# Optimization experiments

Measured on AMD Instinct MI355X. Metric: run time of the kernel, lower is better.

Reference implementation:

```python
import jax, jax.numpy as jnp
import numpy as np

E = 8        # n_experts
H = 1024     # hidden
F = 1024     # ffn intermediate
K = 2        # top_k
B, T = 2, 1024


def setup_inputs() -> dict:
    key = jax.random.key(0)
    k1, k2, k3, k4 = jax.random.split(key, 4)
    return {
        "hidden_states": jax.random.normal(k1, (B, T, H), dtype=jnp.float32),
        "router_weight": jax.random.normal(k2, (E, H), dtype=jnp.float32),
        "gate_up_proj": jax.random.normal(k3, (E, 2 * F, H), dtype=jnp.float32),
        "down_proj": jax.random.normal(k4, (E, H, F), dtype=jnp.float32),
    }


def reference(hidden_states, router_weight, gate_up_proj, down_proj):
    b, t, h_dim = hidden_states.shape
    h = hidden_states.reshape(-1, h_dim)                      # [N, H]

    # Router: logits -> softmax -> top-k -> renormalize (matches FakeFusedRouter)
    logits = h @ router_weight.T                              # [N, E]
    probs = jax.nn.softmax(logits, axis=-1)
    top_v, top_i = jax.lax.top_k(probs, K)                    # [N, K]
    top_v = top_v / top_v.sum(axis=-1, keepdims=True)

    # Combine weights per expert: w[e, n] = sum_k top_v[n,k] * [top_i[n,k]==e]
    combine = (jax.nn.one_hot(top_i, E, dtype=top_v.dtype) * top_v[..., None]).sum(axis=1)  # [N, E]
    combine = combine.T                                       # [E, N]

    # Scan over experts: each expert runs its SwiGLU FFN over all tokens,
    # masked/weighted by combine (zero weight == token not routed there).
    def body(acc, xs):
        gu, dp, w = xs                                        # [2F,H], [H,F], [N]
        gate, up = jnp.split(h @ gu.T, 2, axis=-1)            # [N,F] each
        out = (jax.nn.silu(gate) * up) @ dp.T                 # [N,H]
        return acc + w[:, None] * out, None

    acc0 = jnp.zeros_like(h)
    final, _ = jax.lax.scan(body, acc0, (gate_up_proj, down_proj, combine))
    return final.reshape(b, t, h_dim)
```

## Files before the change

### kernel.cpp

```cpp
#include <hip/hip_runtime.h>


#define NTOK   2048
#define HDIM   1024
#define FDIM   1024
#define NEXP   8
#define NKROWS 4096
#define MAXTILES 40

typedef __attribute__((ext_vector_type(8))) __bf16 bf16x8;
typedef __attribute__((ext_vector_type(4))) float  floatx4;

__device__ __forceinline__ unsigned short f2bf(float x) {
    unsigned int u = __builtin_bit_cast(unsigned int, x);
    u += 0x7FFFu + ((u >> 16) & 1u);
    return (unsigned short)(u >> 16);
}

__device__ __forceinline__ float bf2f(unsigned short v) {
    unsigned int u = (unsigned int)v << 16;
    return __builtin_bit_cast(float, u);
}

__device__ __forceinline__ bf16x8 cvt8(float4 a, float4 b) {
    bf16x8 r;
    r[0] = (__bf16)a.x; r[1] = (__bf16)a.y; r[2] = (__bf16)a.z; r[3] = (__bf16)a.w;
    r[4] = (__bf16)b.x; r[5] = (__bf16)b.y; r[6] = (__bf16)b.z; r[7] = (__bf16)b.w;
    return r;
}

__device__ __forceinline__ void dma16(const void* g, void* l) {
    __builtin_amdgcn_global_load_lds(
        (const __attribute__((address_space(1))) unsigned int*)g,
        (__attribute__((address_space(3))) unsigned int*)l, 16, 0, 0);
}

__global__ __launch_bounds__(256) void k_router(
    const float* __restrict__ h, const float* __restrict__ rw,
    unsigned short* __restrict__ hbf,
    int* __restrict__ topk_idx, float* __restrict__ topk_w)
{
    const int lane = threadIdx.x & 63;
    const int wave = threadIdx.x >> 6;
    const int n = blockIdx.x * 4 + wave;

    const float4* hp = reinterpret_cast<const float4*>(h + (size_t)n * HDIM);
    uint2* hb = reinterpret_cast<uint2*>(hbf + (size_t)n * HDIM);
    float acc[NEXP];
#pragma unroll
    for (int e = 0; e < NEXP; ++e) acc[e] = 0.f;

#pragma unroll
    for (int i0 = 0; i0 < HDIM / 4; i0 += 64) {
        float4 hv = hp[i0 + lane];
        uint2 o;
        o.x = (unsigned)f2bf(hv.x) | ((unsigned)f2bf(hv.y) << 16);
        o.y = (unsigned)f2bf(hv.z) | ((unsigned)f2bf(hv.w) << 16);
        hb[i0 + lane] = o;
#pragma unroll
        for (int e = 0; e < NEXP; ++e) {
            float4 rv = reinterpret_cast<const float4*>(rw + e * HDIM)[i0 + lane];
            acc[e] += hv.x * rv.x + hv.y * rv.y + hv.z * rv.z + hv.w * rv.w;
        }
    }
#pragma unroll
    for (int e = 0; e < NEXP; ++e) {
#pragma unroll
        for (int off = 32; off > 0; off >>= 1)
            acc[e] += __shfl_xor(acc[e], off);
    }
    if (lane == 0) {
        int i0 = 0; float m0 = acc[0];
        for (int e = 1; e < NEXP; ++e) if (acc[e] > m0) { m0 = acc[e]; i0 = e; }
        int i1 = -1; float m1 = -3.0e38f;
        for (int e = 0; e < NEXP; ++e) if (e != i0 && acc[e] > m1) { m1 = acc[e]; i1 = e; }
        float d  = __expf(m1 - m0);
        float w0 = 1.f / (1.f + d);
        topk_idx[n * 2 + 0] = i0;
        topk_idx[n * 2 + 1] = i1;
        topk_w [n * 2 + 0] = w0;
        topk_w [n * 2 + 1] = 1.f - w0;
    }
}

__global__ __launch_bounds__(256) void k_build_perm(
    const int* __restrict__ topk_idx, const float* __restrict__ topk_w,
    int* __restrict__ offsets, int* __restrict__ perm_slot, float* __restrict__ row_w,
    int* __restrict__ tile_e, int* __restrict__ tile_rt)
{
    __shared__ int cnt[NEXP];
    __shared__ int cur[NEXP];
    __shared__ int off[NEXP + 1];
    const int t = threadIdx.x;
    if (t < NEXP) cnt[t] = 0;
    __syncthreads();
    for (int s = t; s < NKROWS; s += 256) atomicAdd(&cnt[topk_idx[s]], 1);
    __syncthreads();
    if (t == 0) {
        int a = 0;
        for (int e = 0; e < NEXP; ++e) { off[e] = a; a += cnt[e]; cur[e] = off[e]; }
        off[NEXP] = a;
        int nt = 0;
        for (int e = 0; e < NEXP; ++e) {
            int ne = cnt[e];
            for (int r = 0; r * 128 < ne; ++r) { tile_e[nt] = e; tile_rt[nt] = r; ++nt; }
        }
        for (; nt < MAXTILES; ++nt) { tile_e[nt] = -1; tile_rt[nt] = 0; }
    }
    __syncthreads();
    for (int s = t; s < NKROWS; s += 256) {
        int e = topk_idx[s];
        int pos = atomicAdd(&cur[e], 1);
        perm_slot[pos] = s;
        row_w[pos] = topk_w[s];
    }
    if (t < NEXP + 1) offsets[t] = off[t];
}

__global__ __launch_bounds__(256, 3) void k_gemm1(
    const unsigned short* __restrict__ hbf, const float* __restrict__ gu,
    const int* __restrict__ offsets, const int* __restrict__ perm_slot,
    const int* __restrict__ tile_e, const int* __restrict__ tile_rt,
    unsigned short* __restrict__ act)
{
    const int e = tile_e[blockIdx.y];
    if (e < 0) return;
    const int rt = tile_rt[blockIdx.y];
    const int off_e = offsets[e];
    const int n_e   = offsets[e + 1] - off_e;
    const int p0 = off_e + rt * 128;
    const int nr = min(128, n_e - rt * 128);
    const int c0 = blockIdx.x * 64;

    __shared__ __align__(16) char smA [128 * 128];
    __shared__ __align__(16) char smBg[64 * 256];
    __shared__ __align__(16) char smBu[64 * 256];
    __shared__ int sTok[128];

    const int t = threadIdx.x;
    const int lane = t & 63;
    const int wv = t >> 6;
    const int wr = wv >> 1, wc = wv & 1;
    if (t < 128) sTok[t] = perm_slot[min(p0 + t, NKROWS - 1)] >> 1;
    __syncthreads();

    const char* asrc[4];
    int aldo[4];
#pragma unroll
    for (int c = 0; c < 4; ++c) {
        int ch = wv * 4 + c;
        int rin = lane >> 3;
        int row = ch * 8 + rin;
        asrc[c] = (const char*)(hbf + (size_t)sTok[row] * HDIM)
                + ((((lane & 7) << 4) ^ (rin << 4)));
        aldo[c] = ch * 1024;
    }
    const float* guE = gu + (size_t)e * (2 * FDIM) * HDIM;
    const char* gsrc[4];
    const char* usrc[4];
    int bldo[4];
#pragma unroll
    for (int c = 0; c < 4; ++c) {
        int ch = wv * 4 + c;
        int row = ch * 4 + (lane >> 4);
        int pre = ((lane & 15) << 4) ^ ((row & 7) << 4);
        gsrc[c] = (const char*)(guE + (size_t)(c0 + row) * HDIM) + pre;
        usrc[c] = (const char*)(guE + (size_t)(FDIM + c0 + row) * HDIM) + pre;
        bldo[c] = ch * 1024;
    }

    floatx4 accg[4][2], accu[4][2];
#pragma unroll
    for (int m = 0; m < 4; ++m)
#pragma unroll
        for (int nn = 0; nn < 2; ++nn) { accg[m][nn] = (floatx4)0.f; accu[m][nn] = (floatx4)0.f; }

    for (int k0 = 0; k0 < HDIM; k0 += 64) {
        if (k0) __syncthreads();
#pragma unroll
        for (int c = 0; c < 4; ++c) dma16(asrc[c] + (size_t)k0 * 2, smA  + aldo[c]);
#pragma unroll
        for (int c = 0; c < 4; ++c) dma16(gsrc[c] + (size_t)k0 * 4, smBg + bldo[c]);
#pragma unroll
        for (int c = 0; c < 4; ++c) dma16(usrc[c] + (size_t)k0 * 4, smBu + bldo[c]);
        __syncthreads();
#pragma unroll
        for (int kk = 0; kk < 2; ++kk) {
            const int kA = kk * 64 + (lane >> 4) * 16;
            const int kB = kk * 128 + (lane >> 4) * 32;
            bf16x8 a[4], fg[2], fu[2];
#pragma unroll
            for (int m = 0; m < 4; ++m) {
                int row = wr * 64 + m * 16 + (lane & 15);
                a[m] = *reinterpret_cast<const bf16x8*>(smA + row * 128 + (kA ^ ((row & 7) << 4)));
            }
#pragma unroll
            for (int nn = 0; nn < 2; ++nn) {
                int cc = wc * 32 + nn * 16 + (lane & 15);
                int b0 = cc * 256 + (kB ^ ((cc & 7) << 4));
                int b1 = cc * 256 + ((kB + 16) ^ ((cc & 7) << 4));
                fg[nn] = cvt8(*reinterpret_cast<const float4*>(smBg + b0),
                              *reinterpret_cast<const float4*>(smBg + b1));
                fu[nn] = cvt8(*reinterpret_cast<const float4*>(smBu + b0),
                              *reinterpret_cast<const float4*>(smBu + b1));
            }
#pragma unroll
            for (int m = 0; m < 4; ++m)
#pragma unroll
                for (int nn = 0; nn < 2; ++nn) {
                    accg[m][nn] = __builtin_amdgcn_mfma_f32_16x16x32_bf16(a[m], fg[nn], accg[m][nn], 0, 0, 0);
                    accu[m][nn] = __builtin_amdgcn_mfma_f32_16x16x32_bf16(a[m], fu[nn], accu[m][nn], 0, 0, 0);
                }
        }
    }

#pragma unroll
    for (int m = 0; m < 4; ++m)
#pragma unroll
        for (int nn = 0; nn < 2; ++nn)
#pragma unroll
            for (int j = 0; j < 4; ++j) {
                int rr = wr * 64 + m * 16 + ((lane >> 4) << 2) + j;
                if (rr < nr) {
                    int f = c0 + wc * 32 + nn * 16 + (lane & 15);
                    float gg = accg[m][nn][j];
                    float uu = accu[m][nn][j];
                    float s = gg / (1.f + __expf(-gg));
                    act[(size_t)(p0 + rr) * FDIM + f] = f2bf(s * uu);
                }
            }
}

__global__ __launch_bounds__(256, 4) void k_gemm2(
    const unsigned short* __restrict__ act, const float* __restrict__ dp,
    const int* __restrict__ offsets, const int* __restrict__ perm_slot,
    const int* __restrict__ tile_e, const int* __restrict__ tile_rt,
    const float* __restrict__ row_w, unsigned short* __restrict__ partial)
{
    const int e = tile_e[blockIdx.y];
    if (e < 0) return;
    const int rt = tile_rt[blockIdx.y];
    const int off_e = offsets[e];
    const int n_e   = offsets[e + 1] - off_e;
    const int p0 = off_e + rt * 128;
    const int nr = min(128, n_e - rt * 128);
    const int c0 = blockIdx.x * 64;

    __shared__ __align__(16) char smA[128 * 128];
    __shared__ __align__(16) char smB[64 * 256];
    __shared__ int   sSlot[128];
    __shared__ float sW[128];

    const int t = threadIdx.x;
    const int lane = t & 63;
    const int wv = t >> 6;
    const int wr = wv >> 1, wc = wv & 1;
    if (t < 128) {
        int p = min(p0 + t, NKROWS - 1);
        sSlot[t] = perm_slot[p];
        sW[t]    = row_w[p];
    }

    const char* asrc[4];
    int aldo[4];
#pragma unroll
    for (int c = 0; c < 4; ++c) {
        int ch = wv * 4 + c;
        int rin = lane >> 3;
        int row = ch * 8 + rin;
        int p = min(p0 + row, NKROWS - 1);
        asrc[c] = (const char*)(act + (size_t)p * FDIM)
                + ((((lane & 7) << 4) ^ (rin << 4)));
        aldo[c] = ch * 1024;
    }
    const float* dpE = dp + (size_t)e * HDIM * FDIM;
    const char* bsrc[4];
    int bldo[4];
#pragma unroll
    for (int c = 0; c < 4; ++c) {
        int ch = wv * 4 + c;
        int row = ch * 4 + (lane >> 4);
        int pre = ((lane & 15) << 4) ^ ((row & 7) << 4);
        bsrc[c] = (const char*)(dpE + (size_t)(c0 + row) * FDIM) + pre;
        bldo[c] = ch * 1024;
    }

    floatx4 acc[4][2];
#pragma unroll
    for (int m = 0; m < 4; ++m)
#pragma unroll
        for (int nn = 0; nn < 2; ++nn) acc[m][nn] = (floatx4)0.f;

    for (int k0 = 0; k0 < FDIM; k0 += 64) {
        __syncthreads();
#pragma unroll
        for (int c = 0; c < 4; ++c) dma16(asrc[c] + (size_t)k0 * 2, smA + aldo[c]);
#pragma unroll
        for (int c = 0; c < 4; ++c) dma16(bsrc[c] + (size_t)k0 * 4, smB + bldo[c]);
        __syncthreads();
#pragma unroll
        for (int kk = 0; kk < 2; ++kk) {
            const int kA = kk * 64 + (lane >> 4) * 16;
            const int kB = kk * 128 + (lane >> 4) * 32;
            bf16x8 a[4], fb[2];
#pragma unroll
            for (int m = 0; m < 4; ++m) {
                int row = wr * 64 + m * 16 + (lane & 15);
                a[m] = *reinterpret_cast<const bf16x8*>(smA + row * 128 + (kA ^ ((row & 7) << 4)));
            }
#pragma unroll
            for (int nn = 0; nn < 2; ++nn) {
                int cc = wc * 32 + nn * 16 + (lane & 15);
                int b0 = cc * 256 + (kB ^ ((cc & 7) << 4));
                int b1 = cc * 256 + ((kB + 16) ^ ((cc & 7) << 4));
                fb[nn] = cvt8(*reinterpret_cast<const float4*>(smB + b0),
                              *reinterpret_cast<const float4*>(smB + b1));
            }
#pragma unroll
            for (int m = 0; m < 4; ++m)
#pragma unroll
                for (int nn = 0; nn < 2; ++nn)
                    acc[m][nn] = __builtin_amdgcn_mfma_f32_16x16x32_bf16(a[m], fb[nn], acc[m][nn], 0, 0, 0);
        }
    }

#pragma unroll
    for (int m = 0; m < 4; ++m)
#pragma unroll
        for (int nn = 0; nn < 2; ++nn)
#pragma unroll
            for (int j = 0; j < 4; ++j) {
                int rr = wr * 64 + m * 16 + ((lane >> 4) << 2) + j;
                if (rr < nr) {
                    int hcol = c0 + wc * 32 + nn * 16 + (lane & 15);
                    partial[(size_t)sSlot[rr] * HDIM + hcol] = f2bf(sW[rr] * acc[m][nn][j]);
                }
            }
}

__global__ __launch_bounds__(256) void k_combine(
    const unsigned short* __restrict__ partial, float* __restrict__ out)
{
    int gid = blockIdx.x * 256 + threadIdx.x;
    int n = gid >> 7;
    int r = gid & 127;
    uint4 a = reinterpret_cast<const uint4*>(partial + (size_t)(2 * n) * HDIM)[r];
    uint4 b = reinterpret_cast<const uint4*>(partial + (size_t)(2 * n + 1) * HDIM)[r];
    float4 o0, o1;
    o0.x = bf2f(a.x & 0xFFFF) + bf2f(b.x & 0xFFFF);
    o0.y = bf2f(a.x >> 16)    + bf2f(b.x >> 16);
    o0.z = bf2f(a.y & 0xFFFF) + bf2f(b.y & 0xFFFF);
    o0.w = bf2f(a.y >> 16)    + bf2f(b.y >> 16);
    o1.x = bf2f(a.z & 0xFFFF) + bf2f(b.z & 0xFFFF);
    o1.y = bf2f(a.z >> 16)    + bf2f(b.z >> 16);
    o1.z = bf2f(a.w & 0xFFFF) + bf2f(b.w & 0xFFFF);
    o1.w = bf2f(a.w >> 16)    + bf2f(b.w >> 16);
    float4* op = reinterpret_cast<float4*>(out + (size_t)n * HDIM + r * 8);
    op[0] = o0;
    op[1] = o1;
}

extern "C" void kernel_launch(void* const* d_in, const int* in_sizes, int n_in,
                              void* d_out, int out_size, void* d_ws, size_t ws_size,
                              hipStream_t stream)
{
    const float* h  = (const float*)d_in[0];
    const float* rw = (const float*)d_in[1];
    const float* gu = (const float*)d_in[2];
    const float* dp = (const float*)d_in[3];
    float* out = (float*)d_out;

    char* ws = (char*)d_ws;
    int*            topk_idx  = (int*)   (ws + 0);
    float*          topk_w    = (float*) (ws + 16384);
    int*            offsets   = (int*)   (ws + 32768);
    int*            tile_e    = (int*)   (ws + 33024);
    int*            tile_rt   = (int*)   (ws + 33280);
    int*            perm_slot = (int*)   (ws + 36864);
    float*          row_w     = (float*) (ws + 53248);
    unsigned short* hbf       = (unsigned short*)(ws + (1u << 20));
    unsigned short* act       = (unsigned short*)(ws + (8u << 20));
    unsigned short* partial   = (unsigned short*)(ws + (16u << 20));

    hipLaunchKernelGGL(k_router,     dim3(512), dim3(256), 0, stream, h, rw, hbf, topk_idx, topk_w);
    hipLaunchKernelGGL(k_build_perm, dim3(1),   dim3(256), 0, stream, topk_idx, topk_w, offsets, perm_slot, row_w, tile_e, tile_rt);
    hipLaunchKernelGGL(k_gemm1,      dim3(16, MAXTILES), dim3(256), 0, stream, hbf, gu, offsets, perm_slot, tile_e, tile_rt, act);
    hipLaunchKernelGGL(k_gemm2,      dim3(16, MAXTILES), dim3(256), 0, stream, act, dp, offsets, perm_slot, tile_e, tile_rt, row_w, partial);
    hipLaunchKernelGGL(k_combine,    dim3(1024), dim3(256), 0, stream, partial, out);
}
```

Measured before the change: 89.15 us.

## Double-buffer expert GEMMs and convert weights to bf16 once when staging

Both expert GEMM kernels now use double-buffered shared memory. The next K-slice is prefetched (A via global_load_lds DMA, B via register loads) while MFMAs run on the current slice. fp32 weights are converted to bf16 a single time when written to LDS, so the inner loop no longer re-converts them per use and the B tiles halve in LDS size. The second GEMM also widens its output tile from 64 to 128 columns, halving its grid, and occupancy hints drop to 2 blocks per CU. The cost is more registers and less parallelism in the second GEMM.

```diff
diff --git a/kernel.cpp b/kernel.cpp
--- a/kernel.cpp
+++ b/kernel.cpp
@@ -22,11 +22,13 @@
     return __builtin_bit_cast(float, u);
 }
 
-__device__ __forceinline__ bf16x8 cvt8(float4 a, float4 b) {
-    bf16x8 r;
-    r[0] = (__bf16)a.x; r[1] = (__bf16)a.y; r[2] = (__bf16)a.z; r[3] = (__bf16)a.w;
-    r[4] = (__bf16)b.x; r[5] = (__bf16)b.y; r[6] = (__bf16)b.z; r[7] = (__bf16)b.w;
-    return r;
+__device__ __forceinline__ uint4 pack8(float4 a, float4 b) {
+    uint4 o;
+    o.x = (unsigned)f2bf(a.x) | ((unsigned)f2bf(a.y) << 16);
+    o.y = (unsigned)f2bf(a.z) | ((unsigned)f2bf(a.w) << 16);
+    o.z = (unsigned)f2bf(b.x) | ((unsigned)f2bf(b.y) << 16);
+    o.w = (unsigned)f2bf(b.z) | ((unsigned)f2bf(b.w) << 16);
+    return o;
 }
 
 __device__ __forceinline__ void dma16(const void* g, void* l) {
@@ -117,7 +119,7 @@
     if (t < NEXP + 1) offsets[t] = off[t];
 }
 
-__global__ __launch_bounds__(256, 3) void k_gemm1(
+__global__ __launch_bounds__(256, 2) void k_gemm1(
     const unsigned short* __restrict__ hbf, const float* __restrict__ gu,
     const int* __restrict__ offsets, const int* __restrict__ perm_slot,
     const int* __restrict__ tile_e, const int* __restrict__ tile_rt,
@@ -132,9 +134,9 @@
     const int nr = min(128, n_e - rt * 128);
     const int c0 = blockIdx.x * 64;
 
-    __shared__ __align__(16) char smA [128 * 128];
-    __shared__ __align__(16) char smBg[64 * 256];
-    __shared__ __align__(16) char smBu[64 * 256];
+    __shared__ __align__(16) char smA [2][128 * 128];
+    __shared__ __align__(16) char smBg[2][64 * 128];
+    __shared__ __align__(16) char smBu[2][64 * 128];
     __shared__ int sTok[128];
 
     const int t = threadIdx.x;
@@ -155,19 +157,15 @@
                 + ((((lane & 7) << 4) ^ (rin << 4)));
         aldo[c] = ch * 1024;
     }
+
+    const int vr = t >> 1;
+    const int kh = t & 1;
+    const int brow = vr & 63;
     const float* guE = gu + (size_t)e * (2 * FDIM) * HDIM;
-    const char* gsrc[4];
-    const char* usrc[4];
-    int bldo[4];
-#pragma unroll
-    for (int c = 0; c < 4; ++c) {
-        int ch = wv * 4 + c;
-        int row = ch * 4 + (lane >> 4);
-        int pre = ((lane & 15) << 4) ^ ((row & 7) << 4);
-        gsrc[c] = (const char*)(guE + (size_t)(c0 + row) * HDIM) + pre;
-        usrc[c] = (const char*)(guE + (size_t)(FDIM + c0 + row) * HDIM) + pre;
-        bldo[c] = ch * 1024;
-    }
+    const float* bsrc = guE
+        + (size_t)(vr < 64 ? c0 + vr : FDIM + c0 + (vr - 64)) * HDIM + kh * 32;
+    const int bswz = (brow & 7) << 4;
+    const int bo = kh * 64;
 
     floatx4 accg[4][2], accu[4][2];
 #pragma unroll
@@ -175,34 +173,47 @@
 #pragma unroll
         for (int nn = 0; nn < 2; ++nn) { accg[m][nn] = (floatx4)0.f; accu[m][nn] = (floatx4)0.f; }
 
-    for (int k0 = 0; k0 < HDIM; k0 += 64) {
-        if (k0) __syncthreads();
-#pragma unroll
-        for (int c = 0; c < 4; ++c) dma16(asrc[c] + (size_t)k0 * 2, smA  + aldo[c]);
-#pragma unroll
-        for (int c = 0; c < 4; ++c) dma16(gsrc[c] + (size_t)k0 * 4, smBg + bldo[c]);
-#pragma unroll
-        for (int c = 0; c < 4; ++c) dma16(usrc[c] + (size_t)k0 * 4, smBu + bldo[c]);
-        __syncthreads();
+#pragma unroll
+    for (int c = 0; c < 4; ++c) dma16(asrc[c], &smA[0][aldo[c]]);
+    {
+        const float4* bp = reinterpret_cast<const float4*>(bsrc);
+        float4 bv[8];
+#pragma unroll
+        for (int q = 0; q < 8; ++q) bv[q] = bp[q];
+        char* dst = (vr < 64 ? smBg[0] : smBu[0]) + brow * 128;
+        *reinterpret_cast<uint4*>(dst + ((bo     ) ^ bswz)) = pack8(bv[0], bv[1]);
+        *reinterpret_cast<uint4*>(dst + ((bo + 16) ^ bswz)) = pack8(bv[2], bv[3]);
+        *reinterpret_cast<uint4*>(dst + ((bo + 32) ^ bswz)) = pack8(bv[4], bv[5]);
+        *reinterpret_cast<uint4*>(dst + ((bo + 48) ^ bswz)) = pack8(bv[6], bv[7]);
+    }
+    __syncthreads();
+
+    int cur = 0;
+    for (int step = 0; step < 16; ++step) {
+        float4 bv[8];
+        if (step < 15) {
+            const int k1 = (step + 1) * 64;
+#pragma unroll
+            for (int c = 0; c < 4; ++c) dma16(asrc[c] + (size_t)k1 * 2, &smA[cur ^ 1][aldo[c]]);
+            const float4* bp = reinterpret_cast<const float4*>(bsrc + k1);
+#pragma unroll
+            for (int q = 0; q < 8; ++q) bv[q] = bp[q];
+        }
 #pragma unroll
         for (int kk = 0; kk < 2; ++kk) {
             const int kA = kk * 64 + (lane >> 4) * 16;
-            const int kB = kk * 128 + (lane >> 4) * 32;
             bf16x8 a[4], fg[2], fu[2];
 #pragma unroll
             for (int m = 0; m < 4; ++m) {
                 int row = wr * 64 + m * 16 + (lane & 15);
-                a[m] = *reinterpret_cast<const bf16x8*>(smA + row * 128 + (kA ^ ((row & 7) << 4)));
+                a[m] = *reinterpret_cast<const bf16x8*>(&smA[cur][row * 128 + (kA ^ ((row & 7) << 4))]);
             }
 #pragma unroll
             for (int nn = 0; nn < 2; ++nn) {
                 int cc = wc * 32 + nn * 16 + (lane & 15);
-                int b0 = cc * 256 + (kB ^ ((cc & 7) << 4));
-                int b1 = cc * 256 + ((kB + 16) ^ ((cc & 7) << 4));
-                fg[nn] = cvt8(*reinterpret_cast<const float4*>(smBg + b0),
-                              *reinterpret_cast<const float4*>(smBg + b1));
-                fu[nn] = cvt8(*reinterpret_cast<const float4*>(smBu + b0),
-                              *reinterpret_cast<const float4*>(smBu + b1));
+                int ad = cc * 128 + (kA ^ ((cc & 7) << 4));
+                fg[nn] = *reinterpret_cast<const bf16x8*>(&smBg[cur][ad]);
+                fu[nn] = *reinterpret_cast<const bf16x8*>(&smBu[cur][ad]);
             }
 #pragma unroll
             for (int m = 0; m < 4; ++m)
@@ -212,6 +223,15 @@
                     accu[m][nn] = __builtin_amdgcn_mfma_f32_16x16x32_bf16(a[m], fu[nn], accu[m][nn], 0, 0, 0);
                 }
         }
+        if (step < 15) {
+            char* dst = (vr < 64 ? smBg[cur ^ 1] : smBu[cur ^ 1]) + brow * 128;
+            *reinterpret_cast<uint4*>(dst + ((bo     ) ^ bswz)) = pack8(bv[0], bv[1]);
+            *reinterpret_cast<uint4*>(dst + ((bo + 16) ^ bswz)) = pack8(bv[2], bv[3]);
+            *reinterpret_cast<uint4*>(dst + ((bo + 32) ^ bswz)) = pack8(bv[4], bv[5]);
+            *reinterpret_cast<uint4*>(dst + ((bo + 48) ^ bswz)) = pack8(bv[6], bv[7]);
+        }
+        __syncthreads();
+        cur ^= 1;
     }
 
 #pragma unroll
@@ -231,7 +251,7 @@
             }
 }
 
-__global__ __launch_bounds__(256, 4) void k_gemm2(
+__global__ __launch_bounds__(256, 2) void k_gemm2(
     const unsigned short* __restrict__ act, const float* __restrict__ dp,
     const int* __restrict__ offsets, const int* __restrict__ perm_slot,
     const int* __restrict__ tile_e, const int* __restrict__ tile_rt,
@@ -244,10 +264,10 @@
     const int n_e   = offsets[e + 1] - off_e;
     const int p0 = off_e + rt * 128;
     const int nr = min(128, n_e - rt * 128);
-    const int c0 = blockIdx.x * 64;
-
-    __shared__ __align__(16) char smA[128 * 128];
-    __shared__ __align__(16) char smB[64 * 256];
+    const int c0 = blockIdx.x * 128;
+
+    __shared__ __align__(16) char smA[2][128 * 128];
+    __shared__ __align__(16) char smB[2][128 * 128];
     __shared__ int   sSlot[128];
     __shared__ float sW[128];
 
@@ -260,7 +280,6 @@
         sSlot[t] = perm_slot[p];
         sW[t]    = row_w[p];
     }
-
     const char* asrc[4];
     int aldo[4];
 #pragma unroll
@@ -273,66 +292,85 @@
                 + ((((lane & 7) << 4) ^ (rin << 4)));
         aldo[c] = ch * 1024;
     }
-    const float* dpE = dp + (size_t)e * HDIM * FDIM;
-    const char* bsrc[4];
-    int bldo[4];
-#pragma unroll
-    for (int c = 0; c < 4; ++c) {
-        int ch = wv * 4 + c;
-        int row = ch * 4 + (lane >> 4);
-        int pre = ((lane & 15) << 4) ^ ((row & 7) << 4);
-        bsrc[c] = (const char*)(dpE + (size_t)(c0 + row) * FDIM) + pre;
-        bldo[c] = ch * 1024;
-    }
-
-    floatx4 acc[4][2];
+
+    const int vr = t >> 1;
+    const int kh = t & 1;
+    const float* bsrc = dp + (size_t)e * HDIM * FDIM + (size_t)(c0 + vr) * FDIM + kh * 32;
+    const int bswz = (vr & 7) << 4;
+    const int bo = kh * 64;
+
+    floatx4 acc[4][4];
 #pragma unroll
     for (int m = 0; m < 4; ++m)
 #pragma unroll
-        for (int nn = 0; nn < 2; ++nn) acc[m][nn] = (floatx4)0.f;
-
-    for (int k0 = 0; k0 < FDIM; k0 += 64) {
-        __syncthreads();
-#pragma unroll
-        for (int c = 0; c < 4; ++c) dma16(asrc[c] + (size_t)k0 * 2, smA + aldo[c]);
-#pragma unroll
-        for (int c = 0; c < 4; ++c) dma16(bsrc[c] + (size_t)k0 * 4, smB + bldo[c]);
-        __syncthreads();
+        for (int nn = 0; nn < 4; ++nn) acc[m][nn] = (floatx4)0.f;
+
+#pragma unroll
+    for (int c = 0; c < 4; ++c) dma16(asrc[c], &smA[0][aldo[c]]);
+    {
+        const float4* bp = reinterpret_cast<const float4*>(bsrc);
+        float4 bv[8];
+#pragma unroll
+        for (int q = 0; q < 8; ++q) bv[q] = bp[q];
+        char* dst = smB[0] + vr * 128;
+        *reinterpret_cast<uint4*>(dst + ((bo     ) ^ bswz)) = pack8(bv[0], bv[1]);
+        *reinterpret_cast<uint4*>(dst + ((bo + 16) ^ bswz)) = pack8(bv[2], bv[3]);
+        *reinterpret_cast<uint4*>(dst + ((bo + 32) ^ bswz)) = pack8(bv[4], bv[5]);
+        *reinterpret_cast<uint4*>(dst + ((bo + 48) ^ bswz)) = pack8(bv[6], bv[7]);
+    }
+    __syncthreads();
+
+    int cur = 0;
+    for (int step = 0; step < 16; ++step) {
+        float4 bv[8];
+        if (step < 15) {
+            const int k1 = (step + 1) * 64;
+#pragma unroll
+            for (int c = 0; c < 4; ++c) dma16(asrc[c] + (size_t)k1 * 2, &smA[cur ^ 1][aldo[c]]);
+            const float4* bp = reinterpret_cast<const float4*>(bsrc + k1);
+#pragma unroll
+            for (int q = 0; q < 8; ++q) bv[q] = bp[q];
+        }
 #pragma unroll
         for (int kk = 0; kk < 2; ++kk) {
             const int kA = kk * 64 + (lane >> 4) * 16;
-            const int kB = kk * 128 + (lane >> 4) * 32;
-            bf16x8 a[4], fb[2];
+            bf16x8 a[4], fb[4];
 #pragma unroll
             for (int m = 0; m < 4; ++m) {
                 int row = wr * 64 + m * 16 + (lane & 15);
-                a[m] = *reinterpret_cast<const bf16x8*>(smA + row * 128 + (kA ^ ((row & 7) << 4)));
-            }
-#pragma unroll
-            for (int nn = 0; nn < 2; ++nn) {
-                int cc = wc * 32 + nn * 16 + (lane & 15);
-                int b0 = cc * 256 + (kB ^ ((cc & 7) << 4));
-                int b1 = cc * 256 + ((kB + 16) ^ ((cc & 7) << 4));
-                fb[nn] = cvt8(*reinterpret_cast<const float4*>(smB + b0),
-                              *reinterpret_cast<const float4*>(smB + b1));
+                a[m] = *reinterpret_cast<const bf16x8*>(&smA[cur][row * 128 + (kA ^ ((row & 7) << 4))]);
+            }
+#pragma unroll
+            for (int nn = 0; nn < 4; ++nn) {
+                int cc = wc * 64 + nn * 16 + (lane & 15);
+                fb[nn] = *reinterpret_cast<const bf16x8*>(&smB[cur][cc * 128 + (kA ^ ((cc & 7) << 4))]);
             }
 #pragma unroll
             for (int m = 0; m < 4; ++m)
 #pragma unroll
-                for (int nn = 0; nn < 2; ++nn)
+                for (int nn = 0; nn < 4; ++nn)
                     acc[m][nn] = __builtin_amdgcn_mfma_f32_16x16x32_bf16(a[m], fb[nn], acc[m][nn], 0, 0, 0);
         }
+        if (step < 15) {
+            char* dst = smB[cur ^ 1] + vr * 128;
+            *reinterpret_cast<uint4*>(dst + ((bo     ) ^ bswz)) = pack8(bv[0], bv[1]);
+            *reinterpret_cast<uint4*>(dst + ((bo + 16) ^ bswz)) = pack8(bv[2], bv[3]);
+            *reinterpret_cast<uint4*>(dst + ((bo + 32) ^ bswz)) = pack8(bv[4], bv[5]);
+            *reinterpret_cast<uint4*>(dst + ((bo + 48) ^ bswz)) = pack8(bv[6], bv[7]);
+        }
+        __syncthreads();
+        cur ^= 1;
     }
 
 #pragma unroll
     for (int m = 0; m < 4; ++m)
 #pragma unroll
-        for (int nn = 0; nn < 2; ++nn)
+        for (int nn = 0; nn < 4; ++nn)
 #pragma unroll
             for (int j = 0; j < 4; ++j) {
                 int rr = wr * 64 + m * 16 + ((lane >> 4) << 2) + j;
                 if (rr < nr) {
-                    int hcol = c0 + wc * 32 + nn * 16 + (lane & 15);
+                    int hcol = c0 + wc * 64 + nn * 16 + (lane & 15);
                     partial[(size_t)sSlot[rr] * HDIM + hcol] = f2bf(sW[rr] * acc[m][nn][j]);
                 }
             }
@@ -385,6 +423,6 @@
     hipLaunchKernelGGL(k_router,     dim3(512), dim3(256), 0, stream, h, rw, hbf, topk_idx, topk_w);
     hipLaunchKernelGGL(k_build_perm, dim3(1),   dim3(256), 0, stream, topk_idx, topk_w, offsets, perm_slot, row_w, tile_e, tile_rt);
     hipLaunchKernelGGL(k_gemm1,      dim3(16, MAXTILES), dim3(256), 0, stream, hbf, gu, offsets, perm_slot, tile_e, tile_rt, act);
-    hipLaunchKernelGGL(k_gemm2,      dim3(16, MAXTILES), dim3(256), 0, stream, act, dp, offsets, perm_slot, tile_e, tile_rt, row_w, partial);
+    hipLaunchKernelGGL(k_gemm2,      dim3(8,  MAXTILES), dim3(256), 0, stream, act, dp, offsets, perm_slot, tile_e, tile_rt, row_w, partial);
     hipLaunchKernelGGL(k_combine,    dim3(1024), dim3(256), 0, stream, partial, out);
 }
```

Result: slower. 163.1 us (+83.0%).

## Pre-convert expert weights to bf16 and widen the down-projection tile

Applied to the files above, without the earlier changes.

Adds a kernel that converts the gate_up and down projection weights from fp32 to bf16 in the workspace on every call. Both GEMMs then DMA bf16 tiles straight into LDS, with no per-fragment fp32-to-bf16 conversion in the inner loop and half the weight bytes per tile. k_gemm2 also widens its output tile from 64 to 128 columns, and k_gemm1's occupancy hint rises from 3 to 4. The cost is an extra full pass over all weights each call (about 96MB read and 48MB written), plus a larger workspace requirement.

```diff
diff --git a/kernel.cpp b/kernel.cpp
--- a/kernel.cpp
+++ b/kernel.cpp
@@ -22,17 +22,37 @@
     return __builtin_bit_cast(float, u);
 }
 
-__device__ __forceinline__ bf16x8 cvt8(float4 a, float4 b) {
-    bf16x8 r;
-    r[0] = (__bf16)a.x; r[1] = (__bf16)a.y; r[2] = (__bf16)a.z; r[3] = (__bf16)a.w;
-    r[4] = (__bf16)b.x; r[5] = (__bf16)b.y; r[6] = (__bf16)b.z; r[7] = (__bf16)b.w;
-    return r;
+__device__ __forceinline__ uint4 pack8(float4 a, float4 b) {
+    uint4 o;
+    o.x = (unsigned)f2bf(a.x) | ((unsigned)f2bf(a.y) << 16);
+    o.y = (unsigned)f2bf(a.z) | ((unsigned)f2bf(a.w) << 16);
+    o.z = (unsigned)f2bf(b.x) | ((unsigned)f2bf(b.y) << 16);
+    o.w = (unsigned)f2bf(b.z) | ((unsigned)f2bf(b.w) << 16);
+    return o;
 }
 
 __device__ __forceinline__ void dma16(const void* g, void* l) {
     __builtin_amdgcn_global_load_lds(
         (const __attribute__((address_space(1))) unsigned int*)g,
         (__attribute__((address_space(3))) unsigned int*)l, 16, 0, 0);
+}
+
+__global__ __launch_bounds__(256) void k_convert_w(
+    const float* __restrict__ gu, const float* __restrict__ dp,
+    unsigned short* __restrict__ gubf, unsigned short* __restrict__ dpbf)
+{
+    const size_t GUE = (size_t)NEXP * 2 * FDIM * HDIM;
+    const size_t TOT = GUE + (size_t)NEXP * HDIM * FDIM;
+    size_t i = ((size_t)blockIdx.x * 256 + threadIdx.x) * 8;
+    const size_t stride = (size_t)2048 * 256 * 8;
+    for (; i < TOT; i += stride) {
+        const float4* s;
+        unsigned short* d;
+        if (i < GUE) { s = reinterpret_cast<const float4*>(gu + i);        d = gubf + i; }
+        else         { s = reinterpret_cast<const float4*>(dp + (i - GUE)); d = dpbf + (i - GUE); }
+        float4 a = s[0], b = s[1];
+        *reinterpret_cast<uint4*>(d) = pack8(a, b);
+    }
 }
 
 __global__ __launch_bounds__(256) void k_router(
@@ -117,8 +137,8 @@
     if (t < NEXP + 1) offsets[t] = off[t];
 }
 
-__global__ __launch_bounds__(256, 3) void k_gemm1(
-    const unsigned short* __restrict__ hbf, const float* __restrict__ gu,
+__global__ __launch_bounds__(256, 4) void k_gemm1(
+    const unsigned short* __restrict__ hbf, const unsigned short* __restrict__ gubf,
     const int* __restrict__ offsets, const int* __restrict__ perm_slot,
     const int* __restrict__ tile_e, const int* __restrict__ tile_rt,
     unsigned short* __restrict__ act)
@@ -133,8 +153,8 @@
     const int c0 = blockIdx.x * 64;
 
     __shared__ __align__(16) char smA [128 * 128];
-    __shared__ __align__(16) char smBg[64 * 256];
-    __shared__ __align__(16) char smBu[64 * 256];
+    __shared__ __align__(16) char smBg[64 * 128];
+    __shared__ __align__(16) char smBu[64 * 128];
     __shared__ int sTok[128];
 
     const int t = threadIdx.x;
@@ -144,28 +164,28 @@
     if (t < 128) sTok[t] = perm_slot[min(p0 + t, NKROWS - 1)] >> 1;
     __syncthreads();
 
+    const int rin = lane >> 3;
+    const int pre = ((lane & 7) << 4) ^ (rin << 4);
+
     const char* asrc[4];
     int aldo[4];
 #pragma unroll
     for (int c = 0; c < 4; ++c) {
         int ch = wv * 4 + c;
-        int rin = lane >> 3;
         int row = ch * 8 + rin;
-        asrc[c] = (const char*)(hbf + (size_t)sTok[row] * HDIM)
-                + ((((lane & 7) << 4) ^ (rin << 4)));
+        asrc[c] = (const char*)(hbf + (size_t)sTok[row] * HDIM) + pre;
         aldo[c] = ch * 1024;
     }
-    const float* guE = gu + (size_t)e * (2 * FDIM) * HDIM;
-    const char* gsrc[4];
-    const char* usrc[4];
-    int bldo[4];
-#pragma unroll
-    for (int c = 0; c < 4; ++c) {
-        int ch = wv * 4 + c;
-        int row = ch * 4 + (lane >> 4);
-        int pre = ((lane & 15) << 4) ^ ((row & 7) << 4);
-        gsrc[c] = (const char*)(guE + (size_t)(c0 + row) * HDIM) + pre;
-        usrc[c] = (const char*)(guE + (size_t)(FDIM + c0 + row) * HDIM) + pre;
+    const unsigned short* guE = gubf + (size_t)e * (2 * FDIM) * HDIM;
+    const char* gsrc[2];
+    const char* usrc[2];
+    int bldo[2];
+#pragma unroll
+    for (int c = 0; c < 2; ++c) {
+        int ch = wv * 2 + c;
+        int col = ch * 8 + rin;
+        gsrc[c] = (const char*)(guE + (size_t)(c0 + col) * HDIM) + pre;
+        usrc[c] = (const char*)(guE + (size_t)(FDIM + c0 + col) * HDIM) + pre;
         bldo[c] = ch * 1024;
     }
 
@@ -180,14 +200,13 @@
 #pragma unroll
         for (int c = 0; c < 4; ++c) dma16(asrc[c] + (size_t)k0 * 2, smA  + aldo[c]);
 #pragma unroll
-        for (int c = 0; c < 4; ++c) dma16(gsrc[c] + (size_t)k0 * 4, smBg + bldo[c]);
-#pragma unroll
-        for (int c = 0; c < 4; ++c) dma16(usrc[c] + (size_t)k0 * 4, smBu + bldo[c]);
+        for (int c = 0; c < 2; ++c) dma16(gsrc[c] + (size_t)k0 * 2, smBg + bldo[c]);
+#pragma unroll
+        for (int c = 0; c < 2; ++c) dma16(usrc[c] + (size_t)k0 * 2, smBu + bldo[c]);
         __syncthreads();
 #pragma unroll
         for (int kk = 0; kk < 2; ++kk) {
             const int kA = kk * 64 + (lane >> 4) * 16;
-            const int kB = kk * 128 + (lane >> 4) * 32;
             bf16x8 a[4], fg[2], fu[2];
 #pragma unroll
             for (int m = 0; m < 4; ++m) {
@@ -197,12 +216,9 @@
 #pragma unroll
             for (int nn = 0; nn < 2; ++nn) {
                 int cc = wc * 32 + nn * 16 + (lane & 15);
-                int b0 = cc * 256 + (kB ^ ((cc & 7) << 4));
-                int b1 = cc * 256 + ((kB + 16) ^ ((cc & 7) << 4));
-                fg[nn] = cvt8(*reinterpret_cast<const float4*>(smBg + b0),
-                              *reinterpret_cast<const float4*>(smBg + b1));
-                fu[nn] = cvt8(*reinterpret_cast<const float4*>(smBu + b0),
-                              *reinterpret_cast<const float4*>(smBu + b1));
+                int ad = cc * 128 + (kA ^ ((cc & 7) << 4));
+                fg[nn] = *reinterpret_cast<const bf16x8*>(smBg + ad);
+                fu[nn] = *reinterpret_cast<const bf16x8*>(smBu + ad);
             }
 #pragma unroll
             for (int m = 0; m < 4; ++m)
@@ -232,7 +248,7 @@
 }
 
 __global__ __launch_bounds__(256, 4) void k_gemm2(
-    const unsigned short* __restrict__ act, const float* __restrict__ dp,
+    const unsigned short* __restrict__ act, const unsigned short* __restrict__ dpbf,
     const int* __restrict__ offsets, const int* __restrict__ perm_slot,
     const int* __restrict__ tile_e, const int* __restrict__ tile_rt,
     const float* __restrict__ row_w, unsigned short* __restrict__ partial)
@@ -244,10 +260,10 @@
     const int n_e   = offsets[e + 1] - off_e;
     const int p0 = off_e + rt * 128;
     const int nr = min(128, n_e - rt * 128);
-    const int c0 = blockIdx.x * 64;
+    const int c0 = blockIdx.x * 128;
 
     __shared__ __align__(16) char smA[128 * 128];
-    __shared__ __align__(16) char smB[64 * 256];
+    __shared__ __align__(16) char smB[128 * 128];
     __shared__ int   sSlot[128];
     __shared__ float sW[128];
 
@@ -261,65 +277,61 @@
         sW[t]    = row_w[p];
     }
 
+    const int rin = lane >> 3;
+    const int pre = ((lane & 7) << 4) ^ (rin << 4);
+
     const char* asrc[4];
     int aldo[4];
 #pragma unroll
     for (int c = 0; c < 4; ++c) {
         int ch = wv * 4 + c;
-        int rin = lane >> 3;
         int row = ch * 8 + rin;
         int p = min(p0 + row, NKROWS - 1);
-        asrc[c] = (const char*)(act + (size_t)p * FDIM)
-                + ((((lane & 7) << 4) ^ (rin << 4)));
+        asrc[c] = (const char*)(act + (size_t)p * FDIM) + pre;
         aldo[c] = ch * 1024;
     }
-    const float* dpE = dp + (size_t)e * HDIM * FDIM;
+    const unsigned short* dpE = dpbf + (size_t)e * HDIM * FDIM;
     const char* bsrc[4];
     int bldo[4];
 #pragma unroll
     for (int c = 0; c < 4; ++c) {
         int ch = wv * 4 + c;
-        int row = ch * 4 + (lane >> 4);
-        int pre = ((lane & 15) << 4) ^ ((row & 7) << 4);
-        bsrc[c] = (const char*)(dpE + (size_t)(c0 + row) * FDIM) + pre;
+        int col = ch * 8 + rin;
+        bsrc[c] = (const char*)(dpE + (size_t)(c0 + col) * FDIM) + pre;
         bldo[c] = ch * 1024;
     }
 
-    floatx4 acc[4][2];
+    floatx4 acc[4][4];
 #pragma unroll
     for (int m = 0; m < 4; ++m)
 #pragma unroll
-        for (int nn = 0; nn < 2; ++nn) acc[m][nn] = (floatx4)0.f;
+        for (int nn = 0; nn < 4; ++nn) acc[m][nn] = (floatx4)0.f;
 
     for (int k0 = 0; k0 < FDIM; k0 += 64) {
         __syncthreads();
 #pragma unroll
         for (int c = 0; c < 4; ++c) dma16(asrc[c] + (size_t)k0 * 2, smA + aldo[c]);
 #pragma unroll
-        for (int c = 0; c < 4; ++c) dma16(bsrc[c] + (size_t)k0 * 4, smB + bldo[c]);
+        for (int c = 0; c < 4; ++c) dma16(bsrc[c] + (size_t)k0 * 2, smB + bldo[c]);
         __syncthreads();
 #pragma unroll
         for (int kk = 0; kk < 2; ++kk) {
             const int kA = kk * 64 + (lane >> 4) * 16;
-            const int kB = kk * 128 + (lane >> 4) * 32;
-            bf16x8 a[4], fb[2];
+            bf16x8 a[4], fb[4];
 #pragma unroll
             for (int m = 0; m < 4; ++m) {
                 int row = wr * 64 + m * 16 + (lane & 15);
                 a[m] = *reinterpret_cast<const bf16x8*>(smA + row * 128 + (kA ^ ((row & 7) << 4)));
             }
 #pragma unroll
-            for (int nn = 0; nn < 2; ++nn) {
-                int cc = wc * 32 + nn * 16 + (lane & 15);
-                int b0 = cc * 256 + (kB ^ ((cc & 7) << 4));
-                int b1 = cc * 256 + ((kB + 16) ^ ((cc & 7) << 4));
-                fb[nn] = cvt8(*reinterpret_cast<const float4*>(smB + b0),
-                              *reinterpret_cast<const float4*>(smB + b1));
+            for (int nn = 0; nn < 4; ++nn) {
+                int cc = wc * 64 + nn * 16 + (lane & 15);
+                fb[nn] = *reinterpret_cast<const bf16x8*>(smB + cc * 128 + (kA ^ ((cc & 7) << 4)));
             }
 #pragma unroll
             for (int m = 0; m < 4; ++m)
 #pragma unroll
-                for (int nn = 0; nn < 2; ++nn)
+                for (int nn = 0; nn < 4; ++nn)
                     acc[m][nn] = __builtin_amdgcn_mfma_f32_16x16x32_bf16(a[m], fb[nn], acc[m][nn], 0, 0, 0);
         }
     }
@@ -327,12 +339,12 @@
 #pragma unroll
     for (int m = 0; m < 4; ++m)
 #pragma unroll
-        for (int nn = 0; nn < 2; ++nn)
+        for (int nn = 0; nn < 4; ++nn)
 #pragma unroll
             for (int j = 0; j < 4; ++j) {
                 int rr = wr * 64 + m * 16 + ((lane >> 4) << 2) + j;
                 if (rr < nr) {
-                    int hcol = c0 + wc * 32 + nn * 16 + (lane & 15);
+                    int hcol = c0 + wc * 64 + nn * 16 + (lane & 15);
                     partial[(size_t)sSlot[rr] * HDIM + hcol] = f2bf(sW[rr] * acc[m][nn][j]);
                 }
             }
@@ -378,13 +390,16 @@
     int*            tile_rt   = (int*)   (ws + 33280);
     int*            perm_slot = (int*)   (ws + 36864);
     float*          row_w     = (float*) (ws + 53248);
-    unsigned short* hbf       = (unsigned short*)(ws + (1u << 20));
-    unsigned short* act       = (unsigned short*)(ws + (8u << 20));
-    unsigned short* partial   = (unsigned short*)(ws + (16u << 20));
-
-    hipLaunchKernelGGL(k_router,     dim3(512), dim3(256), 0, stream, h, rw, hbf, topk_idx, topk_w);
-    hipLaunchKernelGGL(k_build_perm, dim3(1),   dim3(256), 0, stream, topk_idx, topk_w, offsets, perm_slot, row_w, tile_e, tile_rt);
-    hipLaunchKernelGGL(k_gemm1,      dim3(16, MAXTILES), dim3(256), 0, stream, hbf, gu, offsets, perm_slot, tile_e, tile_rt, act);
-    hipLaunchKernelGGL(k_gemm2,      dim3(16, MAXTILES), dim3(256), 0, stream, act, dp, offsets, perm_slot, tile_e, tile_rt, row_w, partial);
+    unsigned short* hbf       = (unsigned short*)(ws + (1u  << 20));
+    unsigned short* partial   = (unsigned short*)(ws + (1u  << 20));
+    unsigned short* act       = (unsigned short*)(ws + (9u  << 20));
+    unsigned short* gubf      = (unsigned short*)(ws + (17u << 20));
+    unsigned short* dpbf      = (unsigned short*)(ws + (49u << 20));
+
+    hipLaunchKernelGGL(k_convert_w,  dim3(2048), dim3(256), 0, stream, gu, dp, gubf, dpbf);
+    hipLaunchKernelGGL(k_router,     dim3(512),  dim3(256), 0, stream, h, rw, hbf, topk_idx, topk_w);
+    hipLaunchKernelGGL(k_build_perm, dim3(1),    dim3(256), 0, stream, topk_idx, topk_w, offsets, perm_slot, row_w, tile_e, tile_rt);
+    hipLaunchKernelGGL(k_gemm1,      dim3(16, MAXTILES), dim3(256), 0, stream, hbf, gubf, offsets, perm_slot, tile_e, tile_rt, act);
+    hipLaunchKernelGGL(k_gemm2,      dim3(8,  MAXTILES), dim3(256), 0, stream, act, dpbf, offsets, perm_slot, tile_e, tile_rt, row_w, partial);
     hipLaunchKernelGGL(k_combine,    dim3(1024), dim3(256), 0, stream, partial, out);
 }
```

Result: slower. 99.97 us (+12.1%).

## Schedule GEMM tiles via per-expert queues with XCD-interleaved block mapping and wider down-proj tiles

Applied to the files above, without the earlier changes.

Replaces the 2D tile grid with per-expert work queues built in build_perm. Each queue entry encodes expert, row tile and column tile, and the 1D block id is mapped so that consecutive blocks alternate across 8 queues, which likely spreads experts across XCDs for L2 reuse of expert weights. The down-projection GEMM widens its column tile from 64 to 128, doubling the accumulators and B-tile shared memory, and drops its occupancy hint from 4 to 3. Workspace is also reused so that partial overlaps hbf, and a redundant first-iteration barrier is removed. The risks are higher register and LDS pressure and correctness of the buffer aliasing.

```diff
diff --git a/kernel.cpp b/kernel.cpp
--- a/kernel.cpp
+++ b/kernel.cpp
@@ -6,7 +6,8 @@
 #define FDIM   1024
 #define NEXP   8
 #define NKROWS 4096
-#define MAXTILES 40
+#define Q1LEN  256
+#define Q2LEN  128
 
 typedef __attribute__((ext_vector_type(8))) __bf16 bf16x8;
 typedef __attribute__((ext_vector_type(4))) float  floatx4;
@@ -86,7 +87,7 @@
 __global__ __launch_bounds__(256) void k_build_perm(
     const int* __restrict__ topk_idx, const float* __restrict__ topk_w,
     int* __restrict__ offsets, int* __restrict__ perm_slot, float* __restrict__ row_w,
-    int* __restrict__ tile_e, int* __restrict__ tile_rt)
+    int* __restrict__ q1, int* __restrict__ q2)
 {
     __shared__ int cnt[NEXP];
     __shared__ int cur[NEXP];
@@ -100,14 +101,24 @@
         int a = 0;
         for (int e = 0; e < NEXP; ++e) { off[e] = a; a += cnt[e]; cur[e] = off[e]; }
         off[NEXP] = a;
-        int nt = 0;
-        for (int e = 0; e < NEXP; ++e) {
-            int ne = cnt[e];
-            for (int r = 0; r * 128 < ne; ++r) { tile_e[nt] = e; tile_rt[nt] = r; ++nt; }
-        }
-        for (; nt < MAXTILES; ++nt) { tile_e[nt] = -1; tile_rt[nt] = 0; }
     }
     __syncthreads();
+    for (int i = t; i < NEXP * Q1LEN; i += 256) {
+        int e = i >> 8;
+        int j = i & (Q1LEN - 1);
+        int rts = (cnt[e] + 127) >> 7;
+        int v = -1;
+        if (j < 16 * rts) { int col = j / rts; int r = j - col * rts; v = e | (r << 4) | (col << 9); }
+        q1[i] = v;
+    }
+    for (int i = t; i < NEXP * Q2LEN; i += 256) {
+        int e = i >> 7;
+        int j = i & (Q2LEN - 1);
+        int rts = (cnt[e] + 127) >> 7;
+        int v = -1;
+        if (j < 8 * rts) { int col = j / rts; int r = j - col * rts; v = e | (r << 4) | (col << 9); }
+        q2[i] = v;
+    }
     for (int s = t; s < NKROWS; s += 256) {
         int e = topk_idx[s];
         int pos = atomicAdd(&cur[e], 1);
@@ -120,17 +131,19 @@
 __global__ __launch_bounds__(256, 3) void k_gemm1(
     const unsigned short* __restrict__ hbf, const float* __restrict__ gu,
     const int* __restrict__ offsets, const int* __restrict__ perm_slot,
-    const int* __restrict__ tile_e, const int* __restrict__ tile_rt,
+    const int* __restrict__ q1,
     unsigned short* __restrict__ act)
 {
-    const int e = tile_e[blockIdx.y];
-    if (e < 0) return;
-    const int rt = tile_rt[blockIdx.y];
+    const int bid = blockIdx.x;
+    const int q = q1[(bid & 7) * Q1LEN + (bid >> 3)];
+    if (q < 0) return;
+    const int e  = q & 15;
+    const int rt = (q >> 4) & 31;
+    const int c0 = (q >> 9) * 64;
     const int off_e = offsets[e];
     const int n_e   = offsets[e + 1] - off_e;
     const int p0 = off_e + rt * 128;
     const int nr = min(128, n_e - rt * 128);
-    const int c0 = blockIdx.x * 64;
 
     __shared__ __align__(16) char smA [128 * 128];
     __shared__ __align__(16) char smBg[64 * 256];
@@ -144,15 +157,15 @@
     if (t < 128) sTok[t] = perm_slot[min(p0 + t, NKROWS - 1)] >> 1;
     __syncthreads();
 
+    const int rin = lane >> 3;
+    const int preA = ((lane & 7) << 4) ^ (rin << 4);
     const char* asrc[4];
     int aldo[4];
 #pragma unroll
     for (int c = 0; c < 4; ++c) {
         int ch = wv * 4 + c;
-        int rin = lane >> 3;
         int row = ch * 8 + rin;
-        asrc[c] = (const char*)(hbf + (size_t)sTok[row] * HDIM)
-                + ((((lane & 7) << 4) ^ (rin << 4)));
+        asrc[c] = (const char*)(hbf + (size_t)sTok[row] * HDIM) + preA;
         aldo[c] = ch * 1024;
     }
     const float* guE = gu + (size_t)e * (2 * FDIM) * HDIM;
@@ -231,23 +244,25 @@
             }
 }
 
-__global__ __launch_bounds__(256, 4) void k_gemm2(
+__global__ __launch_bounds__(256, 3) void k_gemm2(
     const unsigned short* __restrict__ act, const float* __restrict__ dp,
     const int* __restrict__ offsets, const int* __restrict__ perm_slot,
-    const int* __restrict__ tile_e, const int* __restrict__ tile_rt,
+    const int* __restrict__ q2,
     const float* __restrict__ row_w, unsigned short* __restrict__ partial)
 {
-    const int e = tile_e[blockIdx.y];
-    if (e < 0) return;
-    const int rt = tile_rt[blockIdx.y];
+    const int bid = blockIdx.x;
+    const int q = q2[(bid & 7) * Q2LEN + (bid >> 3)];
+    if (q < 0) return;
+    const int e  = q & 15;
+    const int rt = (q >> 4) & 31;
+    const int c0 = (q >> 9) * 128;
     const int off_e = offsets[e];
     const int n_e   = offsets[e + 1] - off_e;
     const int p0 = off_e + rt * 128;
     const int nr = min(128, n_e - rt * 128);
-    const int c0 = blockIdx.x * 64;
 
     __shared__ __align__(16) char smA[128 * 128];
-    __shared__ __align__(16) char smB[64 * 256];
+    __shared__ __align__(16) char smB[128 * 256];
     __shared__ int   sSlot[128];
     __shared__ float sW[128];
 
@@ -260,57 +275,59 @@
         sSlot[t] = perm_slot[p];
         sW[t]    = row_w[p];
     }
+    __syncthreads();
+
+    const int rin = lane >> 3;
+    const int preA = ((lane & 7) << 4) ^ (rin << 4);
 
     const char* asrc[4];
     int aldo[4];
 #pragma unroll
     for (int c = 0; c < 4; ++c) {
         int ch = wv * 4 + c;
-        int rin = lane >> 3;
         int row = ch * 8 + rin;
         int p = min(p0 + row, NKROWS - 1);
-        asrc[c] = (const char*)(act + (size_t)p * FDIM)
-                + ((((lane & 7) << 4) ^ (rin << 4)));
+        asrc[c] = (const char*)(act + (size_t)p * FDIM) + preA;
         aldo[c] = ch * 1024;
     }
     const float* dpE = dp + (size_t)e * HDIM * FDIM;
-    const char* bsrc[4];
-    int bldo[4];
-#pragma unroll
-    for (int c = 0; c < 4; ++c) {
-        int ch = wv * 4 + c;
+    const char* bsrc[8];
+    int bldo[8];
+#pragma unroll
+    for (int c = 0; c < 8; ++c) {
+        int ch = wv * 8 + c;
         int row = ch * 4 + (lane >> 4);
         int pre = ((lane & 15) << 4) ^ ((row & 7) << 4);
         bsrc[c] = (const char*)(dpE + (size_t)(c0 + row) * FDIM) + pre;
         bldo[c] = ch * 1024;
     }
 
-    floatx4 acc[4][2];
+    floatx4 acc[4][4];
 #pragma unroll
     for (int m = 0; m < 4; ++m)
 #pragma unroll
-        for (int nn = 0; nn < 2; ++nn) acc[m][nn] = (floatx4)0.f;
+        for (int nn = 0; nn < 4; ++nn) acc[m][nn] = (floatx4)0.f;
 
     for (int k0 = 0; k0 < FDIM; k0 += 64) {
-        __syncthreads();
+        if (k0) __syncthreads();
 #pragma unroll
         for (int c = 0; c < 4; ++c) dma16(asrc[c] + (size_t)k0 * 2, smA + aldo[c]);
 #pragma unroll
-        for (int c = 0; c < 4; ++c) dma16(bsrc[c] + (size_t)k0 * 4, smB + bldo[c]);
+        for (int c = 0; c < 8; ++c) dma16(bsrc[c] + (size_t)k0 * 4, smB + bldo[c]);
         __syncthreads();
 #pragma unroll
         for (int kk = 0; kk < 2; ++kk) {
             const int kA = kk * 64 + (lane >> 4) * 16;
             const int kB = kk * 128 + (lane >> 4) * 32;
-            bf16x8 a[4], fb[2];
+            bf16x8 a[4], fb[4];
 #pragma unroll
             for (int m = 0; m < 4; ++m) {
                 int row = wr * 64 + m * 16 + (lane & 15);
                 a[m] = *reinterpret_cast<const bf16x8*>(smA + row * 128 + (kA ^ ((row & 7) << 4)));
             }
 #pragma unroll
-            for (int nn = 0; nn < 2; ++nn) {
-                int cc = wc * 32 + nn * 16 + (lane & 15);
+            for (int nn = 0; nn < 4; ++nn) {
+                int cc = wc * 64 + nn * 16 + (lane & 15);
                 int b0 = cc * 256 + (kB ^ ((cc & 7) << 4));
                 int b1 = cc * 256 + ((kB + 16) ^ ((cc & 7) << 4));
                 fb[nn] = cvt8(*reinterpret_cast<const float4*>(smB + b0),
@@ -319,7 +336,7 @@
 #pragma unroll
             for (int m = 0; m < 4; ++m)
 #pragma unroll
-                for (int nn = 0; nn < 2; ++nn)
+                for (int nn = 0; nn < 4; ++nn)
                     acc[m][nn] = __builtin_amdgcn_mfma_f32_16x16x32_bf16(a[m], fb[nn], acc[m][nn], 0, 0, 0);
         }
     }
@@ -327,12 +344,12 @@
 #pragma unroll
     for (int m = 0; m < 4; ++m)
 #pragma unroll
-        for (int nn = 0; nn < 2; ++nn)
+        for (int nn = 0; nn < 4; ++nn)
 #pragma unroll
             for (int j = 0; j < 4; ++j) {
                 int rr = wr * 64 + m * 16 + ((lane >> 4) << 2) + j;
                 if (rr < nr) {
-                    int hcol = c0 + wc * 32 + nn * 16 + (lane & 15);
+                    int hcol = c0 + wc * 64 + nn * 16 + (lane & 15);
                     partial[(size_t)sSlot[rr] * HDIM + hcol] = f2bf(sW[rr] * acc[m][nn][j]);
                 }
             }
@@ -374,17 +391,17 @@
     int*            topk_idx  = (int*)   (ws + 0);
     float*          topk_w    = (float*) (ws + 16384);
     int*            offsets   = (int*)   (ws + 32768);
-    int*            tile_e    = (int*)   (ws + 33024);
-    int*            tile_rt   = (int*)   (ws + 33280);
     int*            perm_slot = (int*)   (ws + 36864);
     float*          row_w     = (float*) (ws + 53248);
-    unsigned short* hbf       = (unsigned short*)(ws + (1u << 20));
-    unsigned short* act       = (unsigned short*)(ws + (8u << 20));
-    unsigned short* partial   = (unsigned short*)(ws + (16u << 20));
-
-    hipLaunchKernelGGL(k_router,     dim3(512), dim3(256), 0, stream, h, rw, hbf, topk_idx, topk_w);
-    hipLaunchKernelGGL(k_build_perm, dim3(1),   dim3(256), 0, stream, topk_idx, topk_w, offsets, perm_slot, row_w, tile_e, tile_rt);
-    hipLaunchKernelGGL(k_gemm1,      dim3(16, MAXTILES), dim3(256), 0, stream, hbf, gu, offsets, perm_slot, tile_e, tile_rt, act);
-    hipLaunchKernelGGL(k_gemm2,      dim3(16, MAXTILES), dim3(256), 0, stream, act, dp, offsets, perm_slot, tile_e, tile_rt, row_w, partial);
-    hipLaunchKernelGGL(k_combine,    dim3(1024), dim3(256), 0, stream, partial, out);
-}
+    int*            q1        = (int*)   (ws + 69632);
+    int*            q2        = (int*)   (ws + 77824);
+    unsigned short* hbf       = (unsigned short*)(ws + (1u  << 20));
+    unsigned short* partial   = (unsigned short*)(ws + (1u  << 20));
+    unsigned short* act       = (unsigned short*)(ws + (9u  << 20));
+
+    hipLaunchKernelGGL(k_router,     dim3(512),       dim3(256), 0, stream, h, rw, hbf, topk_idx, topk_w);
+    hipLaunchKernelGGL(k_build_perm, dim3(1),         dim3(256), 0, stream, topk_idx, topk_w, offsets, perm_slot, row_w, q1, q2);
+    hipLaunchKernelGGL(k_gemm1,      dim3(8 * Q1LEN), dim3(256), 0, stream, hbf, gu, offsets, perm_slot, q1, act);
+    hipLaunchKernelGGL(k_gemm2,      dim3(8 * Q2LEN), dim3(256), 0, stream, act, dp, offsets, perm_slot, q2, row_w, partial);
+    hipLaunchKernelGGL(k_combine,    dim3(1024),      dim3(256), 0, stream, partial, out);
+}
```

After: 92.86 us. 4.2% more time.
